# Optimization experiments

Hardware: AMD Instinct MI355X
Metric: run time of the kernel (lower is better)

## Reference

```python
import jax, jax.numpy as jnp
import numpy as np
import math

SR = 96000.0
FRAME = 2048          # FRAME_SIZE
NB = 16               # N_BIQUADS
B, F = 16, 128        # batch, n_frames
N = F * FRAME         # n_samples (divisible by FRAME)

GAIN_RANGE = (-24.0, 24.0)
BROADBAND = (-60.0, 0.0)
Q_RANGE = (0.5, 16.0)
HPF_R = (20.0, 500.0)
LPF_R = (5000.0, 20000.0)
SHELF_R = (50.0, 16000.0)
PEAK_R = (100.0, 15000.0)


def _denorm_freq(n, r):
    lo, hi = math.log(r[0]), math.log(r[1])
    return jnp.exp(lo + n * (hi - lo))


def _denorm_gain(n, r):
    return r[0] + n * (r[1] - r[0])


def _denorm_q(n):
    lo, hi = math.log(Q_RANGE[0]), math.log(Q_RANGE[1])
    return jnp.exp(lo + n * (hi - lo))


def _norm(b0, b1, b2, a0, a1, a2):
    return b0 / a0, b1 / a0, b2 / a0, a1 / a0, a2 / a0


def _hp(fc, Q):
    w0 = 2 * math.pi * fc / SR
    al = jnp.sin(w0) / (2 * Q)
    c = jnp.cos(w0)
    return _norm((1 + c) / 2, -(1 + c), (1 + c) / 2, 1 + al, -2 * c, 1 - al)


def _lp(fc, Q):
    w0 = 2 * math.pi * fc / SR
    al = jnp.sin(w0) / (2 * Q)
    c = jnp.cos(w0)
    return _norm((1 - c) / 2, 1 - c, (1 - c) / 2, 1 + al, -2 * c, 1 - al)


def _peak(fc, g_db, Q):
    A = jnp.power(10.0, g_db / 40.0)
    w0 = 2 * math.pi * fc / SR
    al = jnp.sin(w0) / (2 * Q)
    c = jnp.cos(w0)
    return _norm(1 + al * A, -2 * c, 1 - al * A, 1 + al / A, -2 * c, 1 - al / A)


def _lowshelf(fc, g_db, Q):
    A = jnp.power(10.0, g_db / 40.0)
    w0 = 2 * math.pi * fc / SR
    al = jnp.sin(w0) / (2 * Q)
    c = jnp.cos(w0)
    sA = jnp.sqrt(A)
    b0 = A * (A + 1 - (A - 1) * c + 2 * sA * al)
    b1 = 2 * A * (A - 1 - (A + 1) * c)
    b2 = A * (A + 1 - (A - 1) * c - 2 * sA * al)
    a0 = A + 1 + (A - 1) * c + 2 * sA * al
    a1 = -2 * (A - 1 + (A + 1) * c)
    a2 = A + 1 + (A - 1) * c - 2 * sA * al
    return _norm(b0, b1, b2, a0, a1, a2)


def _highshelf(fc, g_db, Q):
    A = jnp.power(10.0, g_db / 40.0)
    w0 = 2 * math.pi * fc / SR
    al = jnp.sin(w0) / (2 * Q)
    c = jnp.cos(w0)
    sA = jnp.sqrt(A)
    b0 = A * (A + 1 + (A - 1) * c + 2 * sA * al)
    b1 = -2 * A * (A - 1 + (A + 1) * c)
    b2 = A * (A + 1 + (A - 1) * c - 2 * sA * al)
    a0 = A + 1 - (A - 1) * c + 2 * sA * al
    a1 = 2 * (A - 1 - (A + 1) * c)
    a2 = A + 1 - (A - 1) * c - 2 * sA * al
    return _norm(b0, b1, b2, a0, a1, a2)


def _forward(audio, params):
    b, n = audio.shape
    f = n // FRAME
    fp = params.shape[2]
    # per-audio-frame parameter index: min(frame_idx, n_frames_params-1)
    idx = jnp.minimum(jnp.arange(f), fp - 1)
    p = params[:, :, idx]                       # (B, 50, F)
    bq = p[:, : NB * 3, :].reshape(b, NB, 3, f)  # (B, 16, 3, F)
    in_g = jnp.power(10.0, _denorm_gain(p[:, -2, :], BROADBAND) / 20.0)   # (B,F)
    out_g = jnp.power(10.0, _denorm_gain(p[:, -1, :], BROADBAND) / 20.0)  # (B,F)

    x = audio.reshape(b, f, FRAME) * in_g[:, :, None]

    # per-stage normalized coefficients, each (B, F)
    coefs = []
    for i in range(NB):
        fn, gn, qn = bq[:, i, 0], bq[:, i, 1], bq[:, i, 2]
        Q = _denorm_q(qn)
        if i == 0:                      # BIQUAD_HPF
            c = _hp(_denorm_freq(fn, HPF_R), Q)
        elif i == NB - 1:               # BIQUAD_LPF
            c = _lp(_denorm_freq(fn, LPF_R), Q)
        elif i == 1:                    # BIQUAD_LOW_SHELF
            c = _lowshelf(_denorm_freq(fn, SHELF_R), _denorm_gain(gn, GAIN_RANGE), Q)
        elif i == NB - 2:               # BIQUAD_HIGH_SHELF
            c = _highshelf(_denorm_freq(fn, SHELF_R), _denorm_gain(gn, GAIN_RANGE), Q)
        else:                           # peaking EQ
            c = _peak(_denorm_freq(fn, PEAK_R), _denorm_gain(gn, GAIN_RANGE), Q)
        coefs.append(jnp.stack(c))      # (5, B, F)
    C = jnp.stack(coefs).reshape(NB, 5, b * f)  # (16, 5, B*F)

    # each (batch, frame) lane filters independently with zero initial state
    xt = x.reshape(b * f, FRAME).T              # (T, B*F)

    def step(s, v):
        # s: (16, 2, B*F) DF2T states; v: (B*F,) cascade input
        new_s = []
        for i in range(NB):
            b0, b1, b2, a1, a2 = C[i, 0], C[i, 1], C[i, 2], C[i, 3], C[i, 4]
            y = b0 * v + s[i, 0]
            s1 = b1 * v - a1 * y + s[i, 1]
            s2 = b2 * v - a2 * y
            new_s.append(jnp.stack([s1, s2]))
            v = y
        return jnp.stack(new_s), v

    s0 = jnp.zeros((NB, 2, b * f), dtype=audio.dtype)
    _, ys = jax.lax.scan(step, s0, xt)          # (T, B*F)

    y = ys.T.reshape(b, f, FRAME) * out_g[:, :, None]
    return y.reshape(b, n)


def setup_inputs() -> dict:
    key = jax.random.key(0)
    k1, k2 = jax.random.split(key)
    audio = jax.random.normal(k1, (B, N), dtype=jnp.float32)
    params = jax.random.uniform(k2, (B, 50, F), dtype=jnp.float32)
    return {"audio": audio, "params": params}


def reference(audio, params):
    return _forward(audio, params)
```

## Files before the change

### kernel.cpp

```cpp
#include <hip/hip_runtime.h>
#include <math.h>

namespace {

constexpr int kNB    = 16;
constexpr int kFrame = 2048;
constexpr int kHalf  = 16;

typedef float f32x2 __attribute__((ext_vector_type(2)));

__device__ inline f32x2 pk_fma(f32x2 a, f32x2 b, f32x2 c) {
    f32x2 d;
    asm("v_pk_fma_f32 %0, %1, %2, %3" : "=v"(d) : "v"(a), "v"(b), "v"(c));
    return d;
}
__device__ inline f32x2 pk_mul(f32x2 a, f32x2 b) {
    f32x2 d;
    asm("v_pk_mul_f32 %0, %1, %2" : "=v"(d) : "v"(a), "v"(b));
    return d;
}
__device__ inline f32x2 pk_add(f32x2 a, f32x2 b) {
    f32x2 d;
    asm("v_pk_add_f32 %0, %1, %2" : "=v"(d) : "v"(a), "v"(b));
    return d;
}

template <int CTRL>
__device__ inline float dpp_f(float v) {
    return __int_as_float(
        __builtin_amdgcn_update_dpp(0, __float_as_int(v), CTRL, 0xF, 0xF, true));
}

template <int CTRL>
__device__ inline void ks_level(float& v0, float& v1, const float4 M, const float na1) {
    const float t0 = dpp_f<CTRL>(v0);
    const float t1 = dpp_f<CTRL>(v1);
    const float w  = fmaf(na1, t0, t1);
    v0 = fmaf(M.x, w,  fmaf(M.y, t0, v0));
    v1 = fmaf(M.z, t0, fmaf(M.y, t1, v1));
}

__global__ __launch_bounds__(64)
void biquad_chain_kernel(const float* __restrict__ audio,
                         const float* __restrict__ params,
                         float* __restrict__ out)
{
    __shared__ float4 sK[kNB][2];
    __shared__ float4 powT[kNB][33];

    const int lane = threadIdx.x & 63;
    const int ch   = blockIdx.x;
    const int bb   = ch >> 7;
    const int ff   = ch & 127;

    const float* pb = params + (size_t)bb * (50 * 128) + ff;

    f32x2 X[kHalf];
    {
        const float4* ap = reinterpret_cast<const float4*>(
            audio + (size_t)ch * kFrame + lane * 32);
        #pragma unroll
        for (int k = 0; k < 4; ++k) {
            const float4 va = ap[k];
            const float4 vb = ap[k + 4];
            X[4 * k + 0] = f32x2{va.x, vb.x};
            X[4 * k + 1] = f32x2{va.y, vb.y};
            X[4 * k + 2] = f32x2{va.z, vb.z};
            X[4 * k + 3] = f32x2{va.w, vb.w};
        }
    }

    {
        const int band = lane & 15;
        const int part = lane >> 4;
        const float fn = pb[(band * 3 + 0) * 128];
        const float gn = pb[(band * 3 + 1) * 128];
        const float qn = pb[(band * 3 + 2) * 128];

        const bool isHP = (band == 0), isLP = (band == kNB - 1);
        const bool isShelf = (band == 1) || (band == kNB - 2);
        const float flo = isHP ? 2.995732274f
                        : isLP ? 8.517193191f
                        : isShelf ? 3.912023005f
                        : 4.605170186f;
        const float fsp = isHP ? 3.218875825f
                        : isLP ? 1.386294361f
                        : isShelf ? 5.768320996f
                        : 5.010635294f;

        const float Q  = __expf(fmaf(qn, 3.465735903f, -0.6931471806f));
        const float fc = __expf(fmaf(fn, fsp, flo));
        const float hw = fc * 3.272492349e-5f;
        const float x2 = hw * hw;
        const float sh = hw * fmaf(x2, fmaf(x2, fmaf(x2, -1.984126984e-4f,
                                   8.333333333e-3f), -0.1666666667f), 1.0f);
        const float chh = sqrtf(fmaf(-sh, sh, 1.0f));
        const float sw  = 2.0f * sh * chh;
        const float ver = 2.0f * sh * sh;
        const float alq = sw / (Q + Q);
        const float gdb = (isHP || isLP) ? 0.f : fmaf(gn, 48.f, -24.f);
        const float A   = __expf(gdb * 0.05756462732f);
        const float sA  = sqrtf(A);
        const float ge  = isHP ? fmaf(pb[48 * 128], 60.f, -60.f) * 0.1151292546f
                        : isLP ? fmaf(pb[49 * 128], 60.f, -60.f) * 0.1151292546f
                        : 0.f;
        const float gm  = __expf(ge);

        float b0, b1, b2, a0, a1, a2;
        if (isHP) {
            b0 = 1.0f - 0.5f * ver; b1 = ver - 2.0f; b2 = b0;
            a0 = 1.0f + alq; a1 = 2.0f * ver - 2.0f; a2 = 1.0f - alq;
        } else if (isLP) {
            b0 = 0.5f * ver; b1 = ver; b2 = b0;
            a0 = 1.0f + alq; a1 = 2.0f * ver - 2.0f; a2 = 1.0f - alq;
        } else if (band == 1) {
            const float t = 2.0f * sA * alq;
            const float u = (A - 1.0f) * ver;
            const float w = (A + 1.0f) * ver;
            b0 = A * (2.0f + u + t);
            b1 = A * (2.0f * w - 4.0f);
            b2 = A * (2.0f + u - t);
            a0 = 2.0f * A - u + t;
            a1 = 2.0f * w - 4.0f * A;
            a2 = 2.0f * A - u - t;
        } else if (band == kNB - 2) {
            const float t = 2.0f * sA * alq;
            const float u = (A - 1.0f) * ver;
            const float w = (A + 1.0f) * ver;
            b0 = A * (2.0f * A - u + t);
            b1 = -2.0f * A * (2.0f * A - w);
            b2 = A * (2.0f * A - u - t);
            a0 = 2.0f + u + t;
            a1 = 2.0f * w - 4.0f;
            a2 = 2.0f + u - t;
        } else {
            const float alA  = alq * A;
            const float aloA = alq / A;
            b0 = 1.0f + alA; b1 = 2.0f * ver - 2.0f; b2 = 1.0f - alA;
            a0 = 1.0f + aloA; a1 = b1; a2 = 1.0f - aloA;
        }
        const float inv  = 1.0f / a0;
        const float binv = inv * gm;
        b0 *= binv; b1 *= binv; b2 *= binv;
        a1 *= inv; a2 *= inv;

        const double a1d = (double)a1, a2d = (double)a2;
        double alc = 1.0, bec = 0.0;
        double al16 = 0, be16 = 0, al32 = 0, be32 = 0;
        double al256 = 0, be256 = 0, al512 = 0, be512 = 0;
        #pragma unroll
        for (int k = 1; k <= 9; ++k) {
            const double a_ = alc, b_ = bec;
            alc = a_ * (2.0 * b_ - a1d * a_);
            bec = b_ * b_ - a2d * (a_ * a_);
            if (k == 4) { al16 = alc; be16 = bec; }
            if (k == 5) { al32 = alc; be32 = bec; }
            if (k == 8) { al256 = alc; be256 = bec; }
            if (k == 9) { al512 = alc; be512 = bec; }
        }
        auto cmp = [&](double alx, double bex, double aly, double bey,
                       double& alo, double& beo) {
            const double p = alx * aly;
            alo = alx * bey + bex * aly - a1d * p;
            beo = bex * bey - a2d * p;
        };

        double Sa, Sb;
        if (part == 0)      { Sa = al32; Sb = be32; }
        else if (part == 1) { cmp(al256, be256, al32, be32, Sa, Sb); }
        else if (part == 2) { cmp(al512, be512, al32, be32, Sa, Sb); }
        else { double ta, tb; cmp(al512, be512, al256, be256, ta, tb);
               cmp(ta, tb, al32, be32, Sa, Sb); }

        #pragma unroll
        for (int j = 0; j < 8; ++j) {
            powT[band][8 * part + j] =
                float4{(float)Sa, (float)Sb, (float)(-a2d * Sa), 0.f};
            double na, nb;
            cmp(Sa, Sb, al32, be32, na, nb);
            Sa = na; Sb = nb;
        }
        if (part == 0) {
            sK[band][0] = float4{b0, b1, b2, -a1};
            sK[band][1] = float4{-a2, (float)al16, (float)be16,
                                 (float)(-a2d * al16)};
        }
    }
    __syncthreads();

    for (int band = 0; band < kNB; ++band) {
        const float4 k0 = sK[band][0];
        const float4 k1 = sK[band][1];
        const float4 P1 = powT[band][0];
        const float4 P2 = powT[band][1];
        const float4 P4 = powT[band][3];
        const float4 P8 = powT[band][7];
        const float4 Pme = powT[band][lane & 15];
        const float4 Qme = powT[band][lane & 31];

        const float b0 = k0.x, b1 = k0.y, b2 = k0.z, na1 = k0.w;
        const float na2 = k1.x, al16 = k1.y, be16 = k1.z, ga16 = k1.w;
        const f32x2 b0p  = {b0, b0},  b1p = {b1, b1}, b2p = {b2, b2};
        const f32x2 na1p = {na1, na1}, na2p = {na2, na2};

        f32x2 s1 = {0.f, 0.f}, s2 = {0.f, 0.f};
        #pragma unroll
        for (int t = 0; t < kHalf; ++t) {
            const f32x2 xv = X[t];
            const f32x2 y  = pk_fma(b0p, xv, s1);
            const f32x2 tm = pk_fma(b1p, xv, s2);
            s2 = pk_fma(na2p, y, pk_mul(b2p, xv));
            s1 = pk_fma(na1p, y, tm);
            X[t] = y;
        }

        const float wf = fmaf(na1, s1.x, s2.x);
        const float d0 = fmaf(al16, wf, fmaf(be16, s1.x, s1.y));
        const float d1 = fmaf(ga16, s1.x, fmaf(be16, s2.x, s2.y));

        float v0 = dpp_f<0x138>(d0);
        float v1 = dpp_f<0x138>(d1);
        ks_level<0x111>(v0, v1, P1, na1);
        ks_level<0x112>(v0, v1, P2, na1);
        ks_level<0x114>(v0, v1, P4, na1);
        ks_level<0x118>(v0, v1, P8, na1);
        {
            float t0 = dpp_f<0x142>(v0);
            float t1 = dpp_f<0x142>(v1);
            const bool g = (lane & 16) != 0;
            t0 = g ? t0 : 0.f;
            t1 = g ? t1 : 0.f;
            const float w = fmaf(na1, t0, t1);
            v0 = fmaf(Pme.x, w,  fmaf(Pme.y, t0, v0));
            v1 = fmaf(Pme.z, t0, fmaf(Pme.y, t1, v1));
        }
        {
            float t0 = dpp_f<0x143>(v0);
            float t1 = dpp_f<0x143>(v1);
            const bool g = lane >= 32;
            t0 = g ? t0 : 0.f;
            t1 = g ? t1 : 0.f;
            const float w = fmaf(na1, t0, t1);
            v0 = fmaf(Qme.x, w,  fmaf(Qme.y, t0, v0));
            v1 = fmaf(Qme.z, t0, fmaf(Qme.y, t1, v1));
        }

        const float wr  = fmaf(na1, v0, v1);
        const float uB0 = fmaf(al16, wr, fmaf(be16, v0, s1.x));
        const float uB1 = fmaf(ga16, v0, fmaf(be16, v1, s2.x));

        f32x2 w0 = {v0, uB0}, w1 = {v1, uB1};
        #pragma unroll
        for (int t = 0; t < kHalf; ++t) {
            const f32x2 c = w0;
            X[t] = pk_add(X[t], c);
            w0 = pk_fma(na1p, c, w1);
            w1 = pk_mul(na2p, c);
        }
    }

    {
        float4* op = reinterpret_cast<float4*>(out + (size_t)ch * kFrame + lane * 32);
        #pragma unroll
        for (int k = 0; k < 4; ++k) {
            op[k]     = float4{X[4 * k + 0].x, X[4 * k + 1].x, X[4 * k + 2].x, X[4 * k + 3].x};
            op[k + 4] = float4{X[4 * k + 0].y, X[4 * k + 1].y, X[4 * k + 2].y, X[4 * k + 3].y};
        }
    }
}

}

extern "C" void kernel_launch(void* const* d_in, const int* in_sizes, int n_in,
                              void* d_out, int out_size, void* d_ws, size_t ws_size,
                              hipStream_t stream)
{
    (void)d_ws; (void)ws_size; (void)n_in; (void)in_sizes;
    const float* audio  = (const float*)d_in[0];
    const float* params = (const float*)d_in[1];
    float* outp = (float*)d_out;

    const int channels = out_size / kFrame;
    hipLaunchKernelGGL(biquad_chain_kernel, dim3(channels), dim3(64), 0, stream,
                       audio, params, outp);
}
```

Before: 27.05 us.

## Split each lane's 32 samples into four 8-sample sub-blocks for more ILP

Each lane's 32 samples are now split into four independent 8-sample sub-blocks, processed as two packed-pair chains (P and Q), instead of two 16-sample halves. The per-sample recurrence dependency chain is half as long and two chains are interleaved, which should hide FMA latency with a single wave per block. The cost is extra combine and fixup arithmetic using an 8-step power term (al8/be8) added to the shared table, and more live registers.

After: 27.73 us. +2.5%, slower.

```diff
diff --git a/kernel.cpp b/kernel.cpp
--- a/kernel.cpp
+++ b/kernel.cpp
@@ -5,7 +5,7 @@
 
 constexpr int kNB    = 16;
 constexpr int kFrame = 2048;
-constexpr int kHalf  = 16;
+constexpr int kSub   = 8;
 
 typedef float f32x2 __attribute__((ext_vector_type(2)));
 
@@ -55,19 +55,20 @@
 
     const float* pb = params + (size_t)bb * (50 * 128) + ff;
 
-    f32x2 X[kHalf];
+    f32x2 P[kSub], Q[kSub];
     {
         const float4* ap = reinterpret_cast<const float4*>(
             audio + (size_t)ch * kFrame + lane * 32);
-        #pragma unroll
-        for (int k = 0; k < 4; ++k) {
-            const float4 va = ap[k];
-            const float4 vb = ap[k + 4];
-            X[4 * k + 0] = f32x2{va.x, vb.x};
-            X[4 * k + 1] = f32x2{va.y, vb.y};
-            X[4 * k + 2] = f32x2{va.z, vb.z};
-            X[4 * k + 3] = f32x2{va.w, vb.w};
-        }
+        const float4 f0 = ap[0], f1 = ap[1], f2 = ap[2], f3 = ap[3];
+        const float4 f4 = ap[4], f5 = ap[5], f6 = ap[6], f7 = ap[7];
+        P[0] = f32x2{f0.x, f2.x}; P[1] = f32x2{f0.y, f2.y};
+        P[2] = f32x2{f0.z, f2.z}; P[3] = f32x2{f0.w, f2.w};
+        P[4] = f32x2{f1.x, f3.x}; P[5] = f32x2{f1.y, f3.y};
+        P[6] = f32x2{f1.z, f3.z}; P[7] = f32x2{f1.w, f3.w};
+        Q[0] = f32x2{f4.x, f6.x}; Q[1] = f32x2{f4.y, f6.y};
+        Q[2] = f32x2{f4.z, f6.z}; Q[3] = f32x2{f4.w, f6.w};
+        Q[4] = f32x2{f5.x, f7.x}; Q[5] = f32x2{f5.y, f7.y};
+        Q[6] = f32x2{f5.z, f7.z}; Q[7] = f32x2{f5.w, f7.w};
     }
 
     {
@@ -88,7 +89,7 @@
                         : isShelf ? 5.768320996f
                         : 5.010635294f;
 
-        const float Q  = __expf(fmaf(qn, 3.465735903f, -0.6931471806f));
+        const float Q_  = __expf(fmaf(qn, 3.465735903f, -0.6931471806f));
         const float fc = __expf(fmaf(fn, fsp, flo));
         const float hw = fc * 3.272492349e-5f;
         const float x2 = hw * hw;
@@ -97,7 +98,7 @@
         const float chh = sqrtf(fmaf(-sh, sh, 1.0f));
         const float sw  = 2.0f * sh * chh;
         const float ver = 2.0f * sh * sh;
-        const float alq = sw / (Q + Q);
+        const float alq = sw / (Q_ + Q_);
         const float gdb = (isHP || isLP) ? 0.f : fmaf(gn, 48.f, -24.f);
         const float A   = __expf(gdb * 0.05756462732f);
         const float sA  = sqrtf(A);
@@ -146,6 +147,7 @@
 
         const double a1d = (double)a1, a2d = (double)a2;
         double alc = 1.0, bec = 0.0;
+        double al8 = 0, be8 = 0;
         double al16 = 0, be16 = 0, al32 = 0, be32 = 0;
         double al256 = 0, be256 = 0, al512 = 0, be512 = 0;
         #pragma unroll
@@ -153,6 +155,7 @@
             const double a_ = alc, b_ = bec;
             alc = a_ * (2.0 * b_ - a1d * a_);
             bec = b_ * b_ - a2d * (a_ * a_);
+            if (k == 3) { al8  = alc; be8  = bec; }
             if (k == 4) { al16 = alc; be16 = bec; }
             if (k == 5) { al32 = alc; be32 = bec; }
             if (k == 8) { al256 = alc; be256 = bec; }
@@ -184,6 +187,8 @@
             sK[band][0] = float4{b0, b1, b2, -a1};
             sK[band][1] = float4{-a2, (float)al16, (float)be16,
                                  (float)(-a2d * al16)};
+            powT[band][32] = float4{(float)al8, (float)be8,
+                                    (float)(-a2d * al8), 0.f};
         }
     }
     __syncthreads();
@@ -191,39 +196,54 @@
     for (int band = 0; band < kNB; ++band) {
         const float4 k0 = sK[band][0];
         const float4 k1 = sK[band][1];
-        const float4 P1 = powT[band][0];
-        const float4 P2 = powT[band][1];
-        const float4 P4 = powT[band][3];
-        const float4 P8 = powT[band][7];
+        const float4 K8 = powT[band][32];
+        const float4 P1c = powT[band][0];
+        const float4 P2c = powT[band][1];
+        const float4 P4c = powT[band][3];
+        const float4 P8c = powT[band][7];
         const float4 Pme = powT[band][lane & 15];
         const float4 Qme = powT[band][lane & 31];
 
         const float b0 = k0.x, b1 = k0.y, b2 = k0.z, na1 = k0.w;
         const float na2 = k1.x, al16 = k1.y, be16 = k1.z, ga16 = k1.w;
+        const float al8 = K8.x, be8 = K8.y, ga8 = K8.z;
         const f32x2 b0p  = {b0, b0},  b1p = {b1, b1}, b2p = {b2, b2};
         const f32x2 na1p = {na1, na1}, na2p = {na2, na2};
 
-        f32x2 s1 = {0.f, 0.f}, s2 = {0.f, 0.f};
+        f32x2 s1P = {0.f, 0.f}, s2P = {0.f, 0.f};
+        f32x2 s1Q = {0.f, 0.f}, s2Q = {0.f, 0.f};
         #pragma unroll
-        for (int t = 0; t < kHalf; ++t) {
-            const f32x2 xv = X[t];
-            const f32x2 y  = pk_fma(b0p, xv, s1);
-            const f32x2 tm = pk_fma(b1p, xv, s2);
-            s2 = pk_fma(na2p, y, pk_mul(b2p, xv));
-            s1 = pk_fma(na1p, y, tm);
-            X[t] = y;
-        }
-
-        const float wf = fmaf(na1, s1.x, s2.x);
-        const float d0 = fmaf(al16, wf, fmaf(be16, s1.x, s1.y));
-        const float d1 = fmaf(ga16, s1.x, fmaf(be16, s2.x, s2.y));
+        for (int t = 0; t < kSub; ++t) {
+            const f32x2 xp = P[t];
+            const f32x2 xq = Q[t];
+            const f32x2 yp = pk_fma(b0p, xp, s1P);
+            const f32x2 yq = pk_fma(b0p, xq, s1Q);
+            const f32x2 tp = pk_fma(b1p, xp, s2P);
+            const f32x2 tq = pk_fma(b1p, xq, s2Q);
+            s2P = pk_fma(na2p, yp, pk_mul(b2p, xp));
+            s2Q = pk_fma(na2p, yq, pk_mul(b2p, xq));
+            s1P = pk_fma(na1p, yp, tp);
+            s1Q = pk_fma(na1p, yq, tq);
+            P[t] = yp;
+            Q[t] = yq;
+        }
+
+        const float wp = fmaf(na1, s1P.x, s2P.x);
+        const float d01_0 = fmaf(al8, wp, fmaf(be8, s1P.x, s1P.y));
+        const float d01_1 = fmaf(ga8, s1P.x, fmaf(be8, s2P.x, s2P.y));
+        const float wq = fmaf(na1, s1Q.x, s2Q.x);
+        const float d23_0 = fmaf(al8, wq, fmaf(be8, s1Q.x, s1Q.y));
+        const float d23_1 = fmaf(ga8, s1Q.x, fmaf(be8, s2Q.x, s2Q.y));
+        const float wd = fmaf(na1, d01_0, d01_1);
+        const float d0 = fmaf(al16, wd, fmaf(be16, d01_0, d23_0));
+        const float d1 = fmaf(ga16, d01_0, fmaf(be16, d01_1, d23_1));
 
         float v0 = dpp_f<0x138>(d0);
         float v1 = dpp_f<0x138>(d1);
-        ks_level<0x111>(v0, v1, P1, na1);
-        ks_level<0x112>(v0, v1, P2, na1);
-        ks_level<0x114>(v0, v1, P4, na1);
-        ks_level<0x118>(v0, v1, P8, na1);
+        ks_level<0x111>(v0, v1, P1c, na1);
+        ks_level<0x112>(v0, v1, P2c, na1);
+        ks_level<0x114>(v0, v1, P4c, na1);
+        ks_level<0x118>(v0, v1, P8c, na1);
         {
             float t0 = dpp_f<0x142>(v0);
             float t1 = dpp_f<0x142>(v1);
@@ -246,26 +266,39 @@
         }
 
         const float wr  = fmaf(na1, v0, v1);
-        const float uB0 = fmaf(al16, wr, fmaf(be16, v0, s1.x));
-        const float uB1 = fmaf(ga16, v0, fmaf(be16, v1, s2.x));
-
-        f32x2 w0 = {v0, uB0}, w1 = {v1, uB1};
+        const float u1_0 = fmaf(al8, wr, fmaf(be8, v0, s1P.x));
+        const float u1_1 = fmaf(ga8, v0, fmaf(be8, v1, s2P.x));
+        const float u2_0 = fmaf(al16, wr, fmaf(be16, v0, d01_0));
+        const float u2_1 = fmaf(ga16, v0, fmaf(be16, v1, d01_1));
+        const float wr3  = fmaf(na1, u2_0, u2_1);
+        const float u3_0 = fmaf(al8, wr3, fmaf(be8, u2_0, s1Q.x));
+        const float u3_1 = fmaf(ga8, u2_0, fmaf(be8, u2_1, s2Q.x));
+
+        f32x2 wP0 = {v0, u1_0}, wP1 = {v1, u1_1};
+        f32x2 wQ0 = {u2_0, u3_0}, wQ1 = {u2_1, u3_1};
         #pragma unroll
-        for (int t = 0; t < kHalf; ++t) {
-            const f32x2 c = w0;
-            X[t] = pk_add(X[t], c);
-            w0 = pk_fma(na1p, c, w1);
-            w1 = pk_mul(na2p, c);
+        for (int t = 0; t < kSub; ++t) {
+            const f32x2 cp = wP0;
+            const f32x2 cq = wQ0;
+            P[t] = pk_add(P[t], cp);
+            Q[t] = pk_add(Q[t], cq);
+            wP0 = pk_fma(na1p, cp, wP1);
+            wQ0 = pk_fma(na1p, cq, wQ1);
+            wP1 = pk_mul(na2p, cp);
+            wQ1 = pk_mul(na2p, cq);
         }
     }
 
     {
         float4* op = reinterpret_cast<float4*>(out + (size_t)ch * kFrame + lane * 32);
-        #pragma unroll
-        for (int k = 0; k < 4; ++k) {
-            op[k]     = float4{X[4 * k + 0].x, X[4 * k + 1].x, X[4 * k + 2].x, X[4 * k + 3].x};
-            op[k + 4] = float4{X[4 * k + 0].y, X[4 * k + 1].y, X[4 * k + 2].y, X[4 * k + 3].y};
-        }
+        op[0] = float4{P[0].x, P[1].x, P[2].x, P[3].x};
+        op[1] = float4{P[4].x, P[5].x, P[6].x, P[7].x};
+        op[2] = float4{P[0].y, P[1].y, P[2].y, P[3].y};
+        op[3] = float4{P[4].y, P[5].y, P[6].y, P[7].y};
+        op[4] = float4{Q[0].x, Q[1].x, Q[2].x, Q[3].x};
+        op[5] = float4{Q[4].x, Q[5].x, Q[6].x, Q[7].x};
+        op[6] = float4{Q[0].y, Q[1].y, Q[2].y, Q[3].y};
+        op[7] = float4{Q[4].y, Q[5].y, Q[6].y, Q[7].y};
     }
 }
 
```
